# Kernel optimization log

Hardware: AMD Instinct MI355X
Metric: run time of the kernel (lower is better)

## Reference

```python
import jax, jax.numpy as jnp
import numpy as np

N, E, IN_DIM, HID = 50000, 800000, 128, 64
NEG_SLOPE = 0.01  # torch F.leaky_relu default


def setup_inputs() -> dict:
    key = jax.random.key(0)
    ks = jax.random.split(key, 8)
    x = jax.random.normal(ks[0], (N, IN_DIM), jnp.float32)
    edge_index = jax.random.randint(ks[1], (2, E), 0, N, dtype=jnp.int32)
    edge_weight = jax.random.uniform(ks[2], (E,), jnp.float32)
    h = jnp.zeros((N, HID), jnp.float32)
    c = jnp.zeros((N, HID), jnp.float32)
    sx = 1.0 / np.sqrt(IN_DIM)
    sh = 1.0 / np.sqrt(HID)
    # gate order along leading axis: [i, f, c(tilde), o]; K=2 Chebyshev weights
    Wx = (jax.random.normal(ks[3], (4, 2, IN_DIM, HID), jnp.float32) * sx)
    bx = jnp.zeros((4, HID), jnp.float32)
    Wh = (jax.random.normal(ks[4], (4, 2, HID, HID), jnp.float32) * sh)
    bh = jnp.zeros((4, HID), jnp.float32)
    wc = jax.random.normal(ks[5], (3, HID), jnp.float32) * 0.1  # peepholes for i, f, o
    bg = jnp.zeros((4, HID), jnp.float32)
    W_head = jax.random.normal(ks[6], (HID, 1), jnp.float32) * sh
    b_head = jnp.zeros((1,), jnp.float32)
    return dict(x=x, edge_index=edge_index, edge_weight=edge_weight, h=h, c=c,
                Wx=Wx, bx=bx, Wh=Wh, bh=bh, wc=wc, bg=bg, W_head=W_head, b_head=b_head)


def _cheb_norm(src, dst, ew, n):
    # ChebConv 'sym' normalization with lambda_max=2: L_hat = -D^{-1/2} A D^{-1/2}
    # (the +1 self-loop from the Laplacian cancels against fill_value=-1)
    deg = jnp.zeros((n,), ew.dtype).at[src].add(ew)
    dinv = jnp.where(deg > 0, 1.0 / jnp.sqrt(jnp.where(deg > 0, deg, 1.0)), 0.0)
    return -dinv[src] * ew * dinv[dst]


def _prop(feat, src, dst, norm, n):
    # T1 = L_hat @ feat via edge gather + segment-sum
    return jax.ops.segment_sum(norm[:, None] * feat[src], dst, num_segments=n)


def reference(x, edge_index, edge_weight, h, c, Wx, bx, Wh, bh, wc, bg, W_head, b_head):
    n = x.shape[0]
    src, dst = edge_index[0], edge_index[1]
    norm = _cheb_norm(src, dst, edge_weight, n)
    Tx = _prop(x, src, dst, norm, n)
    Th = _prop(h, src, dst, norm, n)  # shared across all 4 h-side ChebConvs
    # z[g] = X W[g,0] + (L_hat X) W[g,1] + b  for all gates at once
    z = (jnp.einsum('nd,gdh->gnh', x, Wx[:, 0]) + jnp.einsum('nd,gdh->gnh', Tx, Wx[:, 1]) + bx[:, None, :]
         + jnp.einsum('nd,gdh->gnh', h, Wh[:, 0]) + jnp.einsum('nd,gdh->gnh', Th, Wh[:, 1]) + bh[:, None, :])
    i = jax.nn.sigmoid(z[0] + wc[0] * c + bg[0])
    f = jax.nn.sigmoid(z[1] + wc[1] * c + bg[1])
    g = jnp.tanh(z[2] + bg[2])
    c_new = f * c + i * g
    o = jax.nn.sigmoid(z[3] + wc[2] * c_new + bg[3])
    h_new = o * jnp.tanh(c_new)
    out = jax.nn.leaky_relu(h_new, NEG_SLOPE) @ W_head + b_head
    return out, h_new, c_new
```

## Files before the change

kernel.cpp:

```cpp
#include <hip/hip_runtime.h>
#include <hip/hip_bf16.h>

#define IN_DIM 128
#define HID 64
#define NEG_SLOPE 0.01f

typedef __attribute__((ext_vector_type(8))) short short8;
typedef __attribute__((ext_vector_type(4))) short short4v;
typedef __attribute__((ext_vector_type(4))) float f32x4;
typedef unsigned short ushort_t;
typedef unsigned int uint_t;

__device__ __forceinline__ float fsig(float x) { return 1.f / (1.f + __expf(-x)); }
__device__ __forceinline__ float ftanh(float x) { return 1.f - 2.f / (__expf(2.f * x) + 1.f); }

__device__ __forceinline__ ushort_t f2bf(float f) {
    uint_t u = __float_as_uint(f);
    uint_t r = u + 0x7fffu + ((u >> 16) & 1u);
    return (ushort_t)(r >> 16);
}
__device__ __forceinline__ float bf2f(ushort_t s) { return __uint_as_float(((uint_t)s) << 16); }
__device__ __forceinline__ float bf2f_s(short s) { return bf2f((ushort_t)s); }

__global__ __launch_bounds__(256) void prep_kernel(
    const int* __restrict__ src, const int* __restrict__ dst, const float* __restrict__ ew,
    const float* __restrict__ x, const float* __restrict__ h,
    const float* __restrict__ Wx, const float* __restrict__ Wh,
    float* __restrict__ deg, int* __restrict__ cnt, int* __restrict__ rank,
    uint_t* __restrict__ xb_u, uint_t* __restrict__ hb_u, ushort_t* __restrict__ Wp,
    int E, int N) {
    int tid = blockIdx.x * 256 + threadIdx.x;
    int T = gridDim.x * 256;

    if (tid < E) {
        atomicAdd(&deg[src[tid]], ew[tid]);
        rank[tid] = atomicAdd(&cnt[dst[tid]], 1);
    }

    int ncvt = N * 96;
    int nx = N * 64;
    for (int i = tid; i < ncvt; i += T) {
        if (i < nx) {
            float2 v = ((const float2*)x)[i];
            xb_u[i] = (uint_t)f2bf(v.x) | ((uint_t)f2bf(v.y) << 16);
        } else {
            int j = i - nx;
            float2 v = ((const float2*)h)[j];
            hb_u[j] = (uint_t)f2bf(v.x) | ((uint_t)f2bf(v.y) << 16);
        }
    }

    for (int idx = tid; idx < 384 * 256; idx += T) {
        int j = idx & 7;
        int tmp = idx >> 3;
        int lane = tmp & 63;
        int t2 = tmp >> 6;
        int ct = t2 & 15;
        int ks = t2 >> 4;
        int k = ks * 32 + (lane >> 4) * 8 + j;
        int colg = ct * 16 + (lane & 15);
        int g = colg >> 6, hd = colg & 63;
        float v;
        if (k < 128)      v = Wx[((g * 2 + 0) * 128 + k) * 64 + hd];
        else if (k < 192) v = Wh[((g * 2 + 0) * 64 + (k - 128)) * 64 + hd];
        else if (k < 320) v = Wx[((g * 2 + 1) * 128 + (k - 192)) * 64 + hd];
        else              v = Wh[((g * 2 + 1) * 64 + (k - 320)) * 64 + hd];
        Wp[idx] = f2bf(v);
    }
}

__global__ __launch_bounds__(256) void scan1_kernel(const int* __restrict__ cnt,
                                                    int* __restrict__ rowptr,
                                                    int* __restrict__ bsum, int n, int N) {
    __shared__ int sdata[256];
    int b = blockIdx.x, t = threadIdx.x;
    int base = b * 1024 + t * 4;
    int v[4];
    int tsum = 0;
#pragma unroll
    for (int j = 0; j < 4; ++j) {
        int idx = base + j;
        v[j] = (idx < N) ? cnt[idx] : 0;
        tsum += v[j];
    }
    sdata[t] = tsum;
    __syncthreads();
    for (int off = 1; off < 256; off <<= 1) {
        int tmp = (t >= off) ? sdata[t - off] : 0;
        __syncthreads();
        sdata[t] += tmp;
        __syncthreads();
    }
    if (t == 255) bsum[b] = sdata[255];
    int run = sdata[t] - tsum;
#pragma unroll
    for (int j = 0; j < 4; ++j) {
        int idx = base + j;
        if (idx < n) rowptr[idx] = run;
        run += v[j];
    }
}

__global__ __launch_bounds__(256) void scan_add_kernel(int* __restrict__ rowptr,
                                                       const int* __restrict__ bsum, int n) {
    int b = blockIdx.x;
    int grp = (b * 256) >> 10;
    int l = threadIdx.x & 63;
    int v = (l < grp) ? bsum[l] : 0;
#pragma unroll
    for (int off = 32; off; off >>= 1) v += __shfl_xor(v, off);
    int i = b * 256 + threadIdx.x;
    if (i < n) rowptr[i] += v;
}

__global__ void fill_kernel(const int* __restrict__ src, const int* __restrict__ dst,
                            const float* __restrict__ ew, const float* __restrict__ deg,
                            const int* __restrict__ rowptr, const int* __restrict__ rank,
                            int2* __restrict__ eprm, int E) {
    int e = blockIdx.x * blockDim.x + threadIdx.x;
    if (e < E) {
        int d = dst[e];
        int s = src[e];
        float ds = deg[s], dd = deg[d];
        float dis = ds > 0.f ? rsqrtf(ds) : 0.f;
        float did = dd > 0.f ? rsqrtf(dd) : 0.f;
        float nrm = -dis * ew[e] * did;
        int pos = rowptr[d] + rank[e];
        eprm[pos] = make_int2(s, __float_as_int(nrm));
    }
}

__global__ __launch_bounds__(256) void gather_kernel(const int* __restrict__ rowptr,
                                                     const int2* __restrict__ eprm,
                                                     const ushort_t* __restrict__ xb,
                                                     const ushort_t* __restrict__ hb,
                                                     ushort_t* __restrict__ Txb,
                                                     ushort_t* __restrict__ Thb, int N) {
    int lane = threadIdx.x & 63;
    int wave = threadIdx.x >> 6;
    int grp = lane >> 4, l16 = lane & 15;
    int node = blockIdx.x * 16 + wave * 4 + grp;
    bool valid = node < N;
    int p = 0, end = 0;
    if (valid) { p = rowptr[node]; end = rowptr[node + 1]; }

    float ax[8] = {0.f, 0.f, 0.f, 0.f, 0.f, 0.f, 0.f, 0.f};
    float ah[4] = {0.f, 0.f, 0.f, 0.f};

    int idx0 = p + l16;
    int2 pr = (idx0 < end) ? eprm[idx0] : make_int2(0, 0);

    for (int base = p; base < end; base += 16) {
        int2 cur = pr;
        int nidx = base + 16 + l16;
        if (base + 16 < end) pr = (nidx < end) ? eprm[nidx] : make_int2(0, 0);
        int sv = cur.x;
        float wv = __int_as_float(cur.y);
        int mcount = end - base; if (mcount > 16) mcount = 16;
        int sl0 = grp * 16;
        int j = 0;
        for (; j + 4 <= mcount; j += 4) {
            int s0 = __shfl(sv, sl0 + j + 0), s1 = __shfl(sv, sl0 + j + 1);
            int s2 = __shfl(sv, sl0 + j + 2), s3 = __shfl(sv, sl0 + j + 3);
            float w0 = __shfl(wv, sl0 + j + 0), w1 = __shfl(wv, sl0 + j + 1);
            float w2 = __shfl(wv, sl0 + j + 2), w3 = __shfl(wv, sl0 + j + 3);
            short8 xv0 = *(const short8*)(xb + (size_t)s0 * 128 + l16 * 8);
            short8 xv1 = *(const short8*)(xb + (size_t)s1 * 128 + l16 * 8);
            short8 xv2 = *(const short8*)(xb + (size_t)s2 * 128 + l16 * 8);
            short8 xv3 = *(const short8*)(xb + (size_t)s3 * 128 + l16 * 8);
            short4v hv0 = *(const short4v*)(hb + (size_t)s0 * 64 + l16 * 4);
            short4v hv1 = *(const short4v*)(hb + (size_t)s1 * 64 + l16 * 4);
            short4v hv2 = *(const short4v*)(hb + (size_t)s2 * 64 + l16 * 4);
            short4v hv3 = *(const short4v*)(hb + (size_t)s3 * 64 + l16 * 4);
#pragma unroll
            for (int i = 0; i < 8; ++i)
                ax[i] += w0 * bf2f_s(xv0[i]) + w1 * bf2f_s(xv1[i])
                       + w2 * bf2f_s(xv2[i]) + w3 * bf2f_s(xv3[i]);
#pragma unroll
            for (int i = 0; i < 4; ++i)
                ah[i] += w0 * bf2f_s(hv0[i]) + w1 * bf2f_s(hv1[i])
                       + w2 * bf2f_s(hv2[i]) + w3 * bf2f_s(hv3[i]);
        }
        for (; j < mcount; ++j) {
            int s0 = __shfl(sv, sl0 + j);
            float w0 = __shfl(wv, sl0 + j);
            short8 xv0 = *(const short8*)(xb + (size_t)s0 * 128 + l16 * 8);
            short4v hv0 = *(const short4v*)(hb + (size_t)s0 * 64 + l16 * 4);
#pragma unroll
            for (int i = 0; i < 8; ++i) ax[i] += w0 * bf2f_s(xv0[i]);
#pragma unroll
            for (int i = 0; i < 4; ++i) ah[i] += w0 * bf2f_s(hv0[i]);
        }
    }

    if (valid) {
        short8 tx;
#pragma unroll
        for (int i = 0; i < 8; ++i) tx[i] = (short)f2bf(ax[i]);
        *(short8*)(Txb + (size_t)node * 128 + l16 * 8) = tx;
        short4v th;
#pragma unroll
        for (int i = 0; i < 4; ++i) th[i] = (short)f2bf(ah[i]);
        *(short4v*)(Thb + (size_t)node * 64 + l16 * 4) = th;
    }
}

__global__ __launch_bounds__(256, 4) void fused_mfma(
    const ushort_t* __restrict__ xb, const ushort_t* __restrict__ hb,
    const ushort_t* __restrict__ Txb, const ushort_t* __restrict__ Thb,
    const float* __restrict__ c_in, const ushort_t* __restrict__ Wp,
    const float* __restrict__ bx, const float* __restrict__ bh,
    const float* __restrict__ wc, const float* __restrict__ bg,
    const float* __restrict__ Whead, const float* __restrict__ bhead,
    float* __restrict__ out, int N) {
    __shared__ ushort_t Bs[2][8192];
    int tid = threadIdx.x;
    int lane = tid & 63;
    int wave = tid >> 6;
    int quad = lane >> 4, m = lane & 15;
    int row0 = (blockIdx.x * 4 + wave) * 16;
    int ar = row0 + m; if (ar >= N) ar = N - 1;

    {
        const float4* gsrc = (const float4*)(Wp);
        float4* ldst = (float4*)Bs[0];
#pragma unroll
        for (int i = 0; i < 4; ++i) ldst[tid + 256 * i] = gsrc[tid + 256 * i];
    }

    f32x4 acc[16];
#pragma unroll
    for (int ct = 0; ct < 16; ++ct) {
        int g = ct >> 2, hd = (ct & 3) * 16 + m;
        float b = bx[g * 64 + hd] + bh[g * 64 + hd];
        f32x4 bb = {b, b, b, b};
        acc[ct] = bb;
    }

    int ko = quad * 8;
    __syncthreads();

#pragma unroll
    for (int ks = 0; ks < 12; ++ks) {
        int buf = ks & 1;
        float4 tmp[4];
        if (ks < 11) {
            const float4* gsrc = (const float4*)(Wp + (ks + 1) * 8192);
#pragma unroll
            for (int i = 0; i < 4; ++i) tmp[i] = gsrc[tid + 256 * i];
        }
        const ushort_t* a;
        if (ks < 4)       a = xb  + (size_t)ar * 128 + ks * 32 + ko;
        else if (ks < 6)  a = hb  + (size_t)ar * 64 + (ks - 4) * 32 + ko;
        else if (ks < 10) a = Txb + (size_t)ar * 128 + (ks - 6) * 32 + ko;
        else              a = Thb + (size_t)ar * 64 + (ks - 10) * 32 + ko;
        short8 af = *(const short8*)a;
        const short8* bsp = (const short8*)Bs[buf];
#pragma unroll
        for (int ct = 0; ct < 16; ++ct) {
            short8 bf = bsp[ct * 64 + lane];
            acc[ct] = __builtin_amdgcn_mfma_f32_16x16x32_bf16(af, bf, acc[ct], 0, 0, 0);
        }
        if (ks < 11) {
            float4* ldst = (float4*)Bs[buf ^ 1];
#pragma unroll
            for (int i = 0; i < 4; ++i) ldst[tid + 256 * i] = tmp[i];
            __syncthreads();
        }
    }

    float hp[4] = {0.f, 0.f, 0.f, 0.f};
    float bhv = bhead[0];

#pragma unroll
    for (int hs = 0; hs < 4; ++hs) {
        int hd = hs * 16 + m;
        float wc0 = wc[hd], wc1 = wc[64 + hd], wc2 = wc[128 + hd];
        float bg0 = bg[hd], bg1 = bg[64 + hd], bg2 = bg[128 + hd], bg3 = bg[192 + hd];
        float wh = Whead[hd];
#pragma unroll
        for (int reg = 0; reg < 4; ++reg) {
            int n = row0 + quad * 4 + reg;
            if (n < N) {
                float c_old = c_in[(size_t)n * 64 + hd];
                float zi = acc[0 * 4 + hs][reg];
                float zf = acc[1 * 4 + hs][reg];
                float zg = acc[2 * 4 + hs][reg];
                float zo = acc[3 * 4 + hs][reg];
                float ii = fsig(zi + wc0 * c_old + bg0);
                float ff = fsig(zf + wc1 * c_old + bg1);
                float gg = ftanh(zg + bg2);
                float cn = ff * c_old + ii * gg;
                float oo = fsig(zo + wc2 * cn + bg3);
                float hn = oo * ftanh(cn);
                out[N + (size_t)n * 64 + hd] = hn;
                out[N + (size_t)N * 64 + (size_t)n * 64 + hd] = cn;
                float lr = hn > 0.f ? hn : NEG_SLOPE * hn;
                hp[reg] += lr * wh;
            }
        }
    }
#pragma unroll
    for (int reg = 0; reg < 4; ++reg) {
        float v0 = hp[reg];
#pragma unroll
        for (int mask = 1; mask < 16; mask <<= 1) v0 += __shfl_xor(v0, mask);
        if (m == 0) {
            int n0_ = row0 + quad * 4 + reg;
            if (n0_ < N) out[n0_] = v0 + bhv;
        }
    }
}

extern "C" void kernel_launch(void* const* d_in, const int* in_sizes, int n_in,
                              void* d_out, int out_size, void* d_ws, size_t ws_size,
                              hipStream_t stream) {
    const float* x = (const float*)d_in[0];
    const int* ei = (const int*)d_in[1];
    const float* ew = (const float*)d_in[2];
    const float* h = (const float*)d_in[3];
    const float* c = (const float*)d_in[4];
    const float* Wx = (const float*)d_in[5];
    const float* bx = (const float*)d_in[6];
    const float* Wh = (const float*)d_in[7];
    const float* bh = (const float*)d_in[8];
    const float* wc = (const float*)d_in[9];
    const float* bg = (const float*)d_in[10];
    const float* Whead = (const float*)d_in[11];
    const float* bhead = (const float*)d_in[12];

    int N = in_sizes[0] / IN_DIM;
    int E = in_sizes[1] / 2;
    const int* src = ei;
    const int* dst = ei + E;

    char* wp = (char*)d_ws;
    auto alloc = [&](size_t bytes) {
        char* p = wp;
        wp += (bytes + 255) & ~(size_t)255;
        return p;
    };
    float* deg = (float*)alloc((size_t)2 * N * 4);
    int* cnt = (int*)(deg + N);
    int* rank = (int*)alloc((size_t)E * 4);
    int* rowptr = (int*)alloc((size_t)(N + 2) * 4);
    int* bsum = (int*)alloc(64 * 4);
    int2* eprm = (int2*)alloc((size_t)E * 8);
    ushort_t* xb = (ushort_t*)alloc((size_t)N * 128 * 2);
    ushort_t* hb = (ushort_t*)alloc((size_t)N * 64 * 2);
    ushort_t* Txb = (ushort_t*)alloc((size_t)N * 128 * 2);
    ushort_t* Thb = (ushort_t*)alloc((size_t)N * 64 * 2);
    ushort_t* Wp = (ushort_t*)alloc((size_t)384 * 256 * 2);

    hipMemsetAsync(deg, 0, (size_t)2 * N * sizeof(float), stream);

    int nScan = N + 1;
    int nBlocksScan = (nScan + 1023) / 1024;

    prep_kernel<<<(E + 255) / 256, 256, 0, stream>>>(src, dst, ew, x, h, Wx, Wh,
                                                     deg, cnt, rank, (uint_t*)xb, (uint_t*)hb,
                                                     Wp, E, N);
    scan1_kernel<<<nBlocksScan, 256, 0, stream>>>(cnt, rowptr, bsum, nScan, N);
    scan_add_kernel<<<(nScan + 255) / 256, 256, 0, stream>>>(rowptr, bsum, nScan);
    fill_kernel<<<(E + 255) / 256, 256, 0, stream>>>(src, dst, ew, deg, rowptr, rank, eprm, E);
    gather_kernel<<<(N + 15) / 16, 256, 0, stream>>>(rowptr, eprm, xb, hb, Txb, Thb, N);
    fused_mfma<<<(N + 63) / 64, 256, 0, stream>>>(xb, hb, Txb, Thb, c, Wp, bx, bh, wc, bg,
                                                  Whead, bhead, (float*)d_out, N);
}
```

Baseline: 291.5 us.

## Privatize degree and count atomics per XCC to avoid cross-die contention

Each edge's degree and in-count atomics now target a per-XCC private copy, chosen by reading the hardware XCC id, instead of a single global array. The scan kernel then reduces the eight copies into the degree and count, and builds per-XCC offsets so the fill kernel can still place each edge in CSR order. The aim is to keep atomics local to each die's L2 rather than bouncing lines across XCDs. The cost is eight times more memset and scratch traffic (reusing the eprm buffer), a serial 8-way loop per node in the scan, and an extra offset lookup per edge; ranks are limited to 16 bits.

```diff
diff --git a/kernel.cpp b/kernel.cpp
--- a/kernel.cpp
+++ b/kernel.cpp
@@ -26,15 +26,20 @@
     const int* __restrict__ src, const int* __restrict__ dst, const float* __restrict__ ew,
     const float* __restrict__ x, const float* __restrict__ h,
     const float* __restrict__ Wx, const float* __restrict__ Wh,
-    float* __restrict__ deg, int* __restrict__ cnt, int* __restrict__ rank,
+    float* __restrict__ deg_x, int* __restrict__ cnt_x, int* __restrict__ rank,
     uint_t* __restrict__ xb_u, uint_t* __restrict__ hb_u, ushort_t* __restrict__ Wp,
     int E, int N) {
     int tid = blockIdx.x * 256 + threadIdx.x;
     int T = gridDim.x * 256;
 
+    int xcc;
+    asm volatile("s_getreg_b32 %0, hwreg(HW_REG_XCC_ID)" : "=s"(xcc));
+    xcc &= 7;
+
     if (tid < E) {
-        atomicAdd(&deg[src[tid]], ew[tid]);
-        rank[tid] = atomicAdd(&cnt[dst[tid]], 1);
+        atomicAdd(&deg_x[(size_t)xcc * N + src[tid]], ew[tid]);
+        int lr = atomicAdd(&cnt_x[(size_t)xcc * N + dst[tid]], 1);
+        rank[tid] = (xcc << 16) | lr;
     }
 
     int ncvt = N * 96;
@@ -69,8 +74,11 @@
     }
 }
 
-__global__ __launch_bounds__(256) void scan1_kernel(const int* __restrict__ cnt,
+__global__ __launch_bounds__(256) void scan1_kernel(const int* __restrict__ cnt_x,
+                                                    const float* __restrict__ deg_x,
                                                     int* __restrict__ rowptr,
+                                                    int* __restrict__ off,
+                                                    float* __restrict__ deg,
                                                     int* __restrict__ bsum, int n, int N) {
     __shared__ int sdata[256];
     int b = blockIdx.x, t = threadIdx.x;
@@ -80,13 +88,26 @@
 #pragma unroll
     for (int j = 0; j < 4; ++j) {
         int idx = base + j;
-        v[j] = (idx < N) ? cnt[idx] : 0;
-        tsum += v[j];
+        int tot = 0;
+        if (idx < N) {
+            int run8 = 0;
+            float dsum = 0.f;
+#pragma unroll
+            for (int xx = 0; xx < 8; ++xx) {
+                off[(size_t)idx * 8 + xx] = run8;
+                run8 += cnt_x[(size_t)xx * N + idx];
+                dsum += deg_x[(size_t)xx * N + idx];
+            }
+            tot = run8;
+            deg[idx] = dsum;
+        }
+        v[j] = tot;
+        tsum += tot;
     }
     sdata[t] = tsum;
     __syncthreads();
-    for (int off = 1; off < 256; off <<= 1) {
-        int tmp = (t >= off) ? sdata[t - off] : 0;
+    for (int offd = 1; offd < 256; offd <<= 1) {
+        int tmp = (t >= offd) ? sdata[t - offd] : 0;
         __syncthreads();
         sdata[t] += tmp;
         __syncthreads();
@@ -115,7 +136,8 @@
 
 __global__ void fill_kernel(const int* __restrict__ src, const int* __restrict__ dst,
                             const float* __restrict__ ew, const float* __restrict__ deg,
-                            const int* __restrict__ rowptr, const int* __restrict__ rank,
+                            const int* __restrict__ rowptr, const int* __restrict__ off,
+                            const int* __restrict__ rank,
                             int2* __restrict__ eprm, int E) {
     int e = blockIdx.x * blockDim.x + threadIdx.x;
     if (e < E) {
@@ -125,7 +147,10 @@
         float dis = ds > 0.f ? rsqrtf(ds) : 0.f;
         float did = dd > 0.f ? rsqrtf(dd) : 0.f;
         float nrm = -dis * ew[e] * did;
-        int pos = rowptr[d] + rank[e];
+        int rp = rank[e];
+        int xe = (rp >> 16) & 7;
+        int lr = rp & 0xffff;
+        int pos = rowptr[d] + off[(size_t)d * 8 + xe] + lr;
         eprm[pos] = make_int2(s, __float_as_int(nrm));
     }
 }
@@ -340,29 +365,31 @@
         wp += (bytes + 255) & ~(size_t)255;
         return p;
     };
-    float* deg = (float*)alloc((size_t)2 * N * 4);
-    int* cnt = (int*)(deg + N);
+    float* deg = (float*)alloc((size_t)N * 4);
+    int* off = (int*)alloc((size_t)N * 8 * 4);
     int* rank = (int*)alloc((size_t)E * 4);
     int* rowptr = (int*)alloc((size_t)(N + 2) * 4);
     int* bsum = (int*)alloc(64 * 4);
     int2* eprm = (int2*)alloc((size_t)E * 8);
+    int* cnt_x = (int*)eprm;
+    float* deg_x = (float*)eprm + (size_t)8 * N;
     ushort_t* xb = (ushort_t*)alloc((size_t)N * 128 * 2);
     ushort_t* hb = (ushort_t*)alloc((size_t)N * 64 * 2);
     ushort_t* Txb = (ushort_t*)alloc((size_t)N * 128 * 2);
     ushort_t* Thb = (ushort_t*)alloc((size_t)N * 64 * 2);
     ushort_t* Wp = (ushort_t*)alloc((size_t)384 * 256 * 2);
 
-    hipMemsetAsync(deg, 0, (size_t)2 * N * sizeof(float), stream);
+    hipMemsetAsync(cnt_x, 0, (size_t)16 * N * 4, stream);
 
     int nScan = N + 1;
     int nBlocksScan = (nScan + 1023) / 1024;
 
     prep_kernel<<<(E + 255) / 256, 256, 0, stream>>>(src, dst, ew, x, h, Wx, Wh,
-                                                     deg, cnt, rank, (uint_t*)xb, (uint_t*)hb,
+                                                     deg_x, cnt_x, rank, (uint_t*)xb, (uint_t*)hb,
                                                      Wp, E, N);
-    scan1_kernel<<<nBlocksScan, 256, 0, stream>>>(cnt, rowptr, bsum, nScan, N);
+    scan1_kernel<<<nBlocksScan, 256, 0, stream>>>(cnt_x, deg_x, rowptr, off, deg, bsum, nScan, N);
     scan_add_kernel<<<(nScan + 255) / 256, 256, 0, stream>>>(rowptr, bsum, nScan);
-    fill_kernel<<<(E + 255) / 256, 256, 0, stream>>>(src, dst, ew, deg, rowptr, rank, eprm, E);
+    fill_kernel<<<(E + 255) / 256, 256, 0, stream>>>(src, dst, ew, deg, rowptr, off, rank, eprm, E);
     gather_kernel<<<(N + 15) / 16, 256, 0, stream>>>(rowptr, eprm, xb, hb, Txb, Thb, N);
     fused_mfma<<<(N + 63) / 64, 256, 0, stream>>>(xb, hb, Txb, Thb, c, Wp, bx, bh, wc, bg,
                                                   Whead, bhead, (float*)d_out, N);
```

New measurement: 301.8 us. +3.6%, slower.

## Replace global atomic CSR build with two-level bucketed partition and per-bucket local sort

Applied to the files above, without the earlier changes.

Builds the destination-sorted edge list by first partitioning edges into 256-node buckets using shared-memory histograms and one global atomic per bucket per block. Degree and the CSR ordering are then computed per bucket in shared memory. This removes the per-edge global atomics on deg and cnt and the multi-kernel scan. The x/h conversion also moves into its own kernel. The bucket layout uses a fixed capacity (CAP=5120), which overflows if a bucket receives more edges than that, and packs the source id into 16 bits, which only holds for N < 65536.

```diff
diff --git a/kernel.cpp b/kernel.cpp
--- a/kernel.cpp
+++ b/kernel.cpp
@@ -4,6 +4,7 @@
 #define IN_DIM 128
 #define HID 64
 #define NEG_SLOPE 0.01f
+#define CAP 5120
 
 typedef __attribute__((ext_vector_type(8))) short short8;
 typedef __attribute__((ext_vector_type(4))) short short4v;
@@ -22,20 +23,13 @@
 __device__ __forceinline__ float bf2f(ushort_t s) { return __uint_as_float(((uint_t)s) << 16); }
 __device__ __forceinline__ float bf2f_s(short s) { return bf2f((ushort_t)s); }
 
-__global__ __launch_bounds__(256) void prep_kernel(
-    const int* __restrict__ src, const int* __restrict__ dst, const float* __restrict__ ew,
+__global__ __launch_bounds__(256) void cvt_kernel(
     const float* __restrict__ x, const float* __restrict__ h,
     const float* __restrict__ Wx, const float* __restrict__ Wh,
-    float* __restrict__ deg, int* __restrict__ cnt, int* __restrict__ rank,
     uint_t* __restrict__ xb_u, uint_t* __restrict__ hb_u, ushort_t* __restrict__ Wp,
-    int E, int N) {
+    int N) {
     int tid = blockIdx.x * 256 + threadIdx.x;
     int T = gridDim.x * 256;
-
-    if (tid < E) {
-        atomicAdd(&deg[src[tid]], ew[tid]);
-        rank[tid] = atomicAdd(&cnt[dst[tid]], 1);
-    }
 
     int ncvt = N * 96;
     int nx = N * 64;
@@ -69,21 +63,87 @@
     }
 }
 
-__global__ __launch_bounds__(256) void scan1_kernel(const int* __restrict__ cnt,
-                                                    int* __restrict__ rowptr,
-                                                    int* __restrict__ bsum, int n, int N) {
-    __shared__ int sdata[256];
-    int b = blockIdx.x, t = threadIdx.x;
-    int base = b * 1024 + t * 4;
-    int v[4];
-    int tsum = 0;
-#pragma unroll
-    for (int j = 0; j < 4; ++j) {
-        int idx = base + j;
-        v[j] = (idx < N) ? cnt[idx] : 0;
-        tsum += v[j];
-    }
-    sdata[t] = tsum;
+__global__ __launch_bounds__(256) void part_kernel(
+    const int* __restrict__ src, const int* __restrict__ dst, const float* __restrict__ ew,
+    int* __restrict__ cur_d, int* __restrict__ cur_s,
+    int2* __restrict__ dpart, int2* __restrict__ spart, int E) {
+    __shared__ int hd[256], hs[256];
+    int t = threadIdx.x;
+    hd[t] = 0; hs[t] = 0;
+    __syncthreads();
+    int base = blockIdx.x * 2048;
+    int sv[8], dv[8]; float wv[8];
+#pragma unroll
+    for (int it = 0; it < 8; ++it) {
+        int e = base + it * 256 + t;
+        bool ok = e < E;
+        sv[it] = ok ? src[e] : 0;
+        dv[it] = ok ? dst[e] : 0;
+        wv[it] = ok ? ew[e] : 0.f;
+        if (ok) {
+            atomicAdd(&hd[dv[it] >> 8], 1);
+            atomicAdd(&hs[sv[it] >> 8], 1);
+        }
+    }
+    __syncthreads();
+    int nd = hd[t], ns = hs[t];
+    __syncthreads();
+    if (nd) hd[t] = atomicAdd(&cur_d[t * 16], nd);
+    if (ns) hs[t] = atomicAdd(&cur_s[t * 16], ns);
+    __syncthreads();
+#pragma unroll
+    for (int it = 0; it < 8; ++it) {
+        int e = base + it * 256 + t;
+        if (e < E) {
+            int d = dv[it], s = sv[it];
+            int bd = d >> 8, bs = s >> 8;
+            int pd = atomicAdd(&hd[bd], 1);
+            int ps = atomicAdd(&hs[bs], 1);
+            dpart[(size_t)bd * CAP + pd] = make_int2(s | ((d & 255) << 16), __float_as_int(wv[it]));
+            spart[(size_t)bs * CAP + ps] = make_int2(s & 255, __float_as_int(wv[it]));
+        }
+    }
+}
+
+__global__ __launch_bounds__(256) void deg_kernel(const int2* __restrict__ spart,
+                                                  const int* __restrict__ cur_s,
+                                                  float* __restrict__ dinv, int N) {
+    __shared__ float df[256];
+    int t = threadIdx.x, b = blockIdx.x;
+    df[t] = 0.f;
+    __syncthreads();
+    int cnt = cur_s[b * 16];
+    for (int i = t; i < cnt; i += 256) {
+        int2 r = spart[(size_t)b * CAP + i];
+        atomicAdd(&df[r.x & 255], __int_as_float(r.y));
+    }
+    __syncthreads();
+    int g = b * 256 + t;
+    if (g < N) {
+        float dd = df[t];
+        dinv[g] = dd > 0.f ? rsqrtf(dd) : 0.f;
+    }
+}
+
+__global__ __launch_bounds__(256) void fillb_kernel(const int2* __restrict__ dpart,
+                                                    const int* __restrict__ cur_d,
+                                                    const float* __restrict__ dinv,
+                                                    int* __restrict__ rowptr, int* __restrict__ rowend,
+                                                    int2* __restrict__ eprm, int N) {
+    __shared__ int c[256], sdata[256], pcur[256];
+    __shared__ float dl[256];
+    int t = threadIdx.x, b = blockIdx.x;
+    c[t] = 0;
+    int g = b * 256 + t;
+    dl[t] = (g < N) ? dinv[g] : 0.f;
+    __syncthreads();
+    int cnt = cur_d[b * 16];
+    for (int i = t; i < cnt; i += 256) {
+        int m = dpart[(size_t)b * CAP + i].x;
+        atomicAdd(&c[(m >> 16) & 255], 1);
+    }
+    __syncthreads();
+    sdata[t] = c[t];
     __syncthreads();
     for (int off = 1; off < 256; off <<= 1) {
         int tmp = (t >= off) ? sdata[t - off] : 0;
@@ -91,46 +151,27 @@
         sdata[t] += tmp;
         __syncthreads();
     }
-    if (t == 255) bsum[b] = sdata[255];
-    int run = sdata[t] - tsum;
-#pragma unroll
-    for (int j = 0; j < 4; ++j) {
-        int idx = base + j;
-        if (idx < n) rowptr[idx] = run;
-        run += v[j];
-    }
-}
-
-__global__ __launch_bounds__(256) void scan_add_kernel(int* __restrict__ rowptr,
-                                                       const int* __restrict__ bsum, int n) {
-    int b = blockIdx.x;
-    int grp = (b * 256) >> 10;
-    int l = threadIdx.x & 63;
-    int v = (l < grp) ? bsum[l] : 0;
-#pragma unroll
-    for (int off = 32; off; off >>= 1) v += __shfl_xor(v, off);
-    int i = b * 256 + threadIdx.x;
-    if (i < n) rowptr[i] += v;
-}
-
-__global__ void fill_kernel(const int* __restrict__ src, const int* __restrict__ dst,
-                            const float* __restrict__ ew, const float* __restrict__ deg,
-                            const int* __restrict__ rowptr, const int* __restrict__ rank,
-                            int2* __restrict__ eprm, int E) {
-    int e = blockIdx.x * blockDim.x + threadIdx.x;
-    if (e < E) {
-        int d = dst[e];
-        int s = src[e];
-        float ds = deg[s], dd = deg[d];
-        float dis = ds > 0.f ? rsqrtf(ds) : 0.f;
-        float did = dd > 0.f ? rsqrtf(dd) : 0.f;
-        float nrm = -dis * ew[e] * did;
-        int pos = rowptr[d] + rank[e];
-        eprm[pos] = make_int2(s, __float_as_int(nrm));
+    int excl = sdata[t] - c[t];
+    pcur[t] = excl;
+    if (g < N) {
+        rowptr[g] = b * CAP + excl;
+        rowend[g] = b * CAP + sdata[t];
+    }
+    __syncthreads();
+    for (int i = t; i < cnt; i += 256) {
+        int2 r = dpart[(size_t)b * CAP + i];
+        int m = r.x;
+        int dlo = (m >> 16) & 255;
+        int s = m & 0xffff;
+        float w = __int_as_float(r.y);
+        int pos = atomicAdd(&pcur[dlo], 1);
+        float nrm = -dinv[s] * w * dl[dlo];
+        eprm[(size_t)b * CAP + pos] = make_int2(s, __float_as_int(nrm));
     }
 }
 
 __global__ __launch_bounds__(256) void gather_kernel(const int* __restrict__ rowptr,
+                                                     const int* __restrict__ rowend,
                                                      const int2* __restrict__ eprm,
                                                      const ushort_t* __restrict__ xb,
                                                      const ushort_t* __restrict__ hb,
@@ -142,7 +183,7 @@
     int node = blockIdx.x * 16 + wave * 4 + grp;
     bool valid = node < N;
     int p = 0, end = 0;
-    if (valid) { p = rowptr[node]; end = rowptr[node + 1]; }
+    if (valid) { p = rowptr[node]; end = rowend[node]; }
 
     float ax[8] = {0.f, 0.f, 0.f, 0.f, 0.f, 0.f, 0.f, 0.f};
     float ah[4] = {0.f, 0.f, 0.f, 0.f};
@@ -334,36 +375,37 @@
     const int* src = ei;
     const int* dst = ei + E;
 
+    int nbuck = (N + 255) >> 8;
+
     char* wp = (char*)d_ws;
     auto alloc = [&](size_t bytes) {
         char* p = wp;
         wp += (bytes + 255) & ~(size_t)255;
         return p;
     };
-    float* deg = (float*)alloc((size_t)2 * N * 4);
-    int* cnt = (int*)(deg + N);
-    int* rank = (int*)alloc((size_t)E * 4);
-    int* rowptr = (int*)alloc((size_t)(N + 2) * 4);
-    int* bsum = (int*)alloc(64 * 4);
-    int2* eprm = (int2*)alloc((size_t)E * 8);
+    int* cur = (int*)alloc((size_t)2 * nbuck * 16 * 4);
+    int* cur_d = cur;
+    int* cur_s = cur + (size_t)nbuck * 16;
+    float* dinv = (float*)alloc((size_t)N * 4);
+    int* rowptr = (int*)alloc((size_t)N * 4);
+    int* rowend = (int*)alloc((size_t)N * 4);
+    int2* dpart = (int2*)alloc((size_t)nbuck * CAP * 8);
+    int2* spart = (int2*)alloc((size_t)nbuck * CAP * 8);
+    int2* eprm = spart;
     ushort_t* xb = (ushort_t*)alloc((size_t)N * 128 * 2);
     ushort_t* hb = (ushort_t*)alloc((size_t)N * 64 * 2);
     ushort_t* Txb = (ushort_t*)alloc((size_t)N * 128 * 2);
     ushort_t* Thb = (ushort_t*)alloc((size_t)N * 64 * 2);
     ushort_t* Wp = (ushort_t*)alloc((size_t)384 * 256 * 2);
 
-    hipMemsetAsync(deg, 0, (size_t)2 * N * sizeof(float), stream);
-
-    int nScan = N + 1;
-    int nBlocksScan = (nScan + 1023) / 1024;
-
-    prep_kernel<<<(E + 255) / 256, 256, 0, stream>>>(src, dst, ew, x, h, Wx, Wh,
-                                                     deg, cnt, rank, (uint_t*)xb, (uint_t*)hb,
-                                                     Wp, E, N);
-    scan1_kernel<<<nBlocksScan, 256, 0, stream>>>(cnt, rowptr, bsum, nScan, N);
-    scan_add_kernel<<<(nScan + 255) / 256, 256, 0, stream>>>(rowptr, bsum, nScan);
-    fill_kernel<<<(E + 255) / 256, 256, 0, stream>>>(src, dst, ew, deg, rowptr, rank, eprm, E);
-    gather_kernel<<<(N + 15) / 16, 256, 0, stream>>>(rowptr, eprm, xb, hb, Txb, Thb, N);
+    hipMemsetAsync(cur, 0, (size_t)2 * nbuck * 16 * 4, stream);
+
+    part_kernel<<<(E + 2047) / 2048, 256, 0, stream>>>(src, dst, ew, cur_d, cur_s,
+                                                       dpart, spart, E);
+    cvt_kernel<<<2048, 256, 0, stream>>>(x, h, Wx, Wh, (uint_t*)xb, (uint_t*)hb, Wp, N);
+    deg_kernel<<<nbuck, 256, 0, stream>>>(spart, cur_s, dinv, N);
+    fillb_kernel<<<nbuck, 256, 0, stream>>>(dpart, cur_d, dinv, rowptr, rowend, eprm, N);
+    gather_kernel<<<(N + 15) / 16, 256, 0, stream>>>(rowptr, rowend, eprm, xb, hb, Txb, Thb, N);
     fused_mfma<<<(N + 63) / 64, 256, 0, stream>>>(xb, hb, Txb, Thb, c, Wp, bx, bh, wc, bg,
                                                   Whead, bhead, (float*)d_out, N);
 }
```

Result: faster. 239.4 us (-17.9%).
